# Performance work log

Hardware: AMD Instinct MI355X
Metric: run time of the kernel (lower is better)

## Reference

```python
import jax, jax.numpy as jnp
import numpy as np

N_NODES = 100000
N_EDGES = 300000
HID = 256
N0, N1, N2 = 40000, 30000, 30000
D0, D1, D2 = 512, 256, 128


def setup_inputs() -> dict:
    key = jax.random.key(0)
    ks = jax.random.split(key, 14)
    s = 0.05  # init scale
    return {
        "feat0": jax.random.normal(ks[0], (N0, D0), jnp.float32),
        "feat1": jax.random.normal(ks[1], (N1, D1), jnp.float32),
        "feat2": jax.random.normal(ks[2], (N2, D2), jnp.float32),
        # per-type Linear(in_dim, HID) params (torch Linear: y = x @ W.T + b)
        "fc_w0": jax.random.normal(ks[3], (HID, D0), jnp.float32) * s,
        "fc_b0": jnp.zeros((HID,), jnp.float32),
        "fc_w1": jax.random.normal(ks[4], (HID, D1), jnp.float32) * s,
        "fc_b1": jnp.zeros((HID,), jnp.float32),
        "fc_w2": jax.random.normal(ks[5], (HID, D2), jnp.float32) * s,
        "fc_b2": jnp.zeros((HID,), jnp.float32),
        # GraphConv 1: weight=False, bias=True
        "gc1_bias": jnp.zeros((HID,), jnp.float32),
        # GraphConv 2: weight (in,out) + bias (DGL convention: feat @ W)
        "gc2_weight": jax.random.normal(ks[6], (HID, HID), jnp.float32) * s,
        "gc2_bias": jnp.zeros((HID,), jnp.float32),
        "semantic_weight": jax.random.normal(ks[7], (1, 5), jnp.float32),
        "src": jax.random.randint(ks[8], (N_EDGES,), 0, N_NODES, jnp.int64),
        "dst": jax.random.randint(ks[9], (N_EDGES,), 0, N_NODES, jnp.int64),
    }


def reference(feat0, feat1, feat2, fc_w0, fc_b0, fc_w1, fc_b1, fc_w2, fc_b2,
              gc1_bias, gc2_weight, gc2_bias, semantic_weight, src, dst):
    # per-type projection then concat along node dim -> [N_NODES, HID]
    h = jnp.concatenate([
        feat0 @ fc_w0.T + fc_b0,
        feat1 @ fc_w1.T + fc_b1,
        feat2 @ fc_w2.T + fc_b2,
    ], axis=0)

    ones = jnp.ones((src.shape[0],), h.dtype)
    deg_out = jnp.maximum(jax.ops.segment_sum(ones, src, num_segments=N_NODES), 1.0)
    deg_in = jnp.maximum(jax.ops.segment_sum(ones, dst, num_segments=N_NODES), 1.0)
    norm_out = jax.lax.rsqrt(deg_out)[:, None]  # D_out^{-1/2}
    norm_in = jax.lax.rsqrt(deg_in)[:, None]    # D_in^{-1/2}

    def gconv(x, W, b):
        # DGL GraphConv, norm='both': D_in^{-1/2} A D_out^{-1/2} x W + b, relu
        msg = (x * norm_out)[src]                                  # [E, HID]
        agg = jax.ops.segment_sum(msg, dst, num_segments=N_NODES)  # [N, HID]
        agg = agg * norm_in
        if W is not None:
            agg = agg @ W
        return jax.nn.relu(agg + b)

    # dropout is identity in eval mode
    h = gconv(h, None, gc1_bias)        # layer 0: weight=False
    h = gconv(h, gc2_weight, gc2_bias)  # layer 1
    return h, semantic_weight
```

## Files before the change

### kernel.cpp

```cpp
#include <hip/hip_runtime.h>
#include <cstdint>

#define HID 256
static constexpr int    NNODES = 100000;
static constexpr int    NEDGES = 300000;
static constexpr size_t NH     = (size_t)NNODES * HID;
static constexpr int    SCAN_B = 256;
static constexpr int    NSBLK  = (NNODES + SCAN_B - 1) / SCAN_B;

typedef __attribute__((ext_vector_type(8))) short bf16x8;
typedef __attribute__((ext_vector_type(4))) float f32x4;

__device__ __forceinline__ unsigned short f2bf(float x) {
    unsigned int u = __float_as_uint(x);
    u += 0x7fffu + ((u >> 16) & 1u);
    return (unsigned short)(u >> 16);
}
__device__ __forceinline__ unsigned int pack2(float a, float b) {
    return (unsigned int)f2bf(a) | ((unsigned int)f2bf(b) << 16);
}
__device__ __forceinline__ float bflo(unsigned int u) { return __uint_as_float(u << 16); }
__device__ __forceinline__ float bfhi(unsigned int u) { return __uint_as_float(u & 0xffff0000u); }

__global__ void zero_i32_k(int* __restrict__ p, int n) {
    int i = blockIdx.x * blockDim.x + threadIdx.x;
    if (i < n) p[i] = 0;
}

__global__ void count_deg_k(const int* __restrict__ src, const int* __restrict__ dst,
                            int* __restrict__ degout, int* __restrict__ degin) {
    int e = blockIdx.x * blockDim.x + threadIdx.x;
    if (e < NEDGES) {
        atomicAdd(degout + src[e], 1);
        atomicAdd(degin  + dst[e], 1);
    }
}

__global__ void cvt_weights_k(const float* __restrict__ w0, const float* __restrict__ w1,
                              const float* __restrict__ w2, const float* __restrict__ wg,
                              unsigned short* __restrict__ o0, unsigned short* __restrict__ o1,
                              unsigned short* __restrict__ o2, unsigned short* __restrict__ ogT) {
    int b = blockIdx.x, t = threadIdx.x;
    const float* in; unsigned short* out; int i;
    if (b < 128)      { in = w0; out = o0; i = b * 256 + t; }
    else if (b < 192) { in = w1; out = o1; i = (b - 128) * 256 + t; }
    else if (b < 224) { in = w2; out = o2; i = (b - 192) * 256 + t; }
    else {
        int n = b - 224, k = t;
        ogT[n * 256 + k] = f2bf(wg[k * 256 + n]);
        return;
    }
    float4 v = ((const float4*)in)[i];
    ushort4 w;
    w.x = f2bf(v.x); w.y = f2bf(v.y); w.z = f2bf(v.z); w.w = f2bf(v.w);
    ((ushort4*)out)[i] = w;
}

__global__ void scan_a_k(const int* __restrict__ degin, const int* __restrict__ degout,
                         int* __restrict__ row_off, int* __restrict__ bsums,
                         float* __restrict__ nout, float* __restrict__ nin,
                         const float* __restrict__ sw, float* __restrict__ tail) {
    __shared__ int sm[SCAN_B];
    int t = threadIdx.x;
    int g = blockIdx.x * SCAN_B + t;
    int v = (g < NNODES) ? degin[g] : 0;
    sm[t] = v;
    if (g < NNODES) {
        nout[g] = rsqrtf(fmaxf((float)degout[g], 1.0f));
        nin[g]  = rsqrtf(fmaxf((float)v, 1.0f));
    }
    if (g < 5) tail[g] = sw[g];
    __syncthreads();
#pragma unroll
    for (int off = 1; off < SCAN_B; off <<= 1) {
        int x = (t >= off) ? sm[t - off] : 0;
        __syncthreads();
        sm[t] += x;
        __syncthreads();
    }
    if (g < NNODES) row_off[g] = sm[t] - v;
    if (t == SCAN_B - 1) bsums[blockIdx.x] = sm[t];
}

__global__ void scan_b_k(int* __restrict__ bsums) {
    __shared__ int sm[512];
    int t = threadIdx.x;
    int v = (t < NSBLK) ? bsums[t] : 0;
    sm[t] = v;
    __syncthreads();
#pragma unroll
    for (int off = 1; off < 512; off <<= 1) {
        int x = (t >= off) ? sm[t - off] : 0;
        __syncthreads();
        sm[t] += x;
        __syncthreads();
    }
    if (t < NSBLK) bsums[t] = sm[t] - v;
}

__global__ void scan_c_k(int* __restrict__ row_off, const int* __restrict__ bsums) {
    int g = blockIdx.x * SCAN_B + threadIdx.x;
    if (g < NNODES) row_off[g] += bsums[blockIdx.x];
    if (g == 0) row_off[NNODES] = NEDGES;
}

__global__ void fill_csr_k(const int* __restrict__ src, const int* __restrict__ dst,
                           const int* __restrict__ row_off, int* __restrict__ cursor,
                           int* __restrict__ csr_src) {
    int e = blockIdx.x * blockDim.x + threadIdx.x;
    if (e < NEDGES) {
        int d = dst[e];
        int pos = row_off[d] + atomicAdd(cursor + d, 1);
        csr_src[pos] = src[e];
    }
}

__global__ __launch_bounds__(256) void gather_bf16_k(
    const unsigned short* __restrict__ h, const int* __restrict__ row_off,
    const int* __restrict__ csr_src, const float* __restrict__ nin,
    const float* __restrict__ nout, const float* __restrict__ bias,
    unsigned short* __restrict__ out)
{
    int node = blockIdx.x * 4 + (threadIdx.x >> 6);
    if (node >= NNODES) return;
    int lane = threadIdx.x & 63;
    int beg = row_off[node], end = row_off[node + 1];
    float a0 = 0.f, a1 = 0.f, a2 = 0.f, a3 = 0.f;
    for (int e = beg; e < end; ++e) {
        int s = csr_src[e];
        uint2 v = *(const uint2*)(h + (size_t)s * HID + lane * 4);
        a0 += bflo(v.x); a1 += bfhi(v.x);
        a2 += bflo(v.y); a3 += bfhi(v.y);
    }
    float ni = nin[node], no = nout[node];
    float4 bb = *(const float4*)(bias + lane * 4);
    a0 = fmaxf(fmaf(a0, ni, bb.x), 0.f) * no;
    a1 = fmaxf(fmaf(a1, ni, bb.y), 0.f) * no;
    a2 = fmaxf(fmaf(a2, ni, bb.z), 0.f) * no;
    a3 = fmaxf(fmaf(a3, ni, bb.w), 0.f) * no;
    ushort4 o;
    o.x = f2bf(a0); o.y = f2bf(a1); o.z = f2bf(a2); o.w = f2bf(a3);
    *(ushort4*)(out + (size_t)node * HID + lane * 4) = o;
}

__global__ __launch_bounds__(256, 3) void proj_mfma_k(
    const float* __restrict__ f0, const float* __restrict__ f1, const float* __restrict__ f2,
    const unsigned short* __restrict__ w0, const unsigned short* __restrict__ w1,
    const unsigned short* __restrict__ w2,
    const float* __restrict__ b0, const float* __restrict__ b1, const float* __restrict__ b2,
    const float* __restrict__ nout, unsigned short* __restrict__ h0)
{
    __shared__ unsigned short As[64 * 32];
    __shared__ unsigned short Bs[256 * 32];

    int bx = blockIdx.x;
    const float* A; const unsigned short* B; const float* bias; const float* rs;
    unsigned short* C; int M, K;
    if (bx < 625)       { A = f0; B = w0; bias = b0; rs = nout;          C = h0;                          M = 40000; K = 512; }
    else if (bx < 1094) { bx -= 625;  A = f1; B = w1; bias = b1; rs = nout + 40000; C = h0 + (size_t)40000 * HID; M = 30000; K = 256; }
    else                { bx -= 1094; A = f2; B = w2; bias = b2; rs = nout + 70000; C = h0 + (size_t)70000 * HID; M = 30000; K = 128; }
    const int m0 = bx * 64;

    const int tid  = threadIdx.x;
    const int wn   = tid >> 6;
    const int lane = tid & 63;
    const int half = lane >> 4;
    const int l15  = lane & 15;

    f32x4 acc[4][4];
#pragma unroll
    for (int i = 0; i < 4; ++i)
#pragma unroll
        for (int j = 0; j < 4; ++j)
#pragma unroll
            for (int r = 0; r < 4; ++r) acc[i][j][r] = 0.f;

    const int arow = tid >> 2, ac = tid & 3;
    const int aslot = ac ^ ((arow >> 1) & 3);
    int agm = m0 + arow; if (agm > M - 1) agm = M - 1;

    for (int k0 = 0; k0 < K; k0 += 32) {
        {
            const float* p = A + (size_t)agm * K + k0 + ac * 8;
            float4 v0 = *(const float4*)p;
            float4 v1 = *(const float4*)(p + 4);
            uint4 u;
            u.x = pack2(v0.x, v0.y); u.y = pack2(v0.z, v0.w);
            u.z = pack2(v1.x, v1.y); u.w = pack2(v1.z, v1.w);
            *(uint4*)&As[(arow * 4 + aslot) * 8] = u;
        }
#pragma unroll
        for (int t = 0; t < 4; ++t) {
            int q = tid + t * 256;
            int row = q >> 2, c = q & 3;
            int slot = c ^ ((row >> 1) & 3);
            uint4 v = *(const uint4*)(B + (size_t)row * K + k0 + c * 8);
            *(uint4*)&Bs[(row * 4 + slot) * 8] = v;
        }
        __syncthreads();

        bf16x8 af[4], bfr[4];
#pragma unroll
        for (int i = 0; i < 4; ++i) {
            int m = i * 16 + l15;
            int ca = half ^ ((m >> 1) & 3);
            af[i] = *(const bf16x8*)&As[(m * 4 + ca) * 8];
            int n = wn * 64 + i * 16 + l15;
            int cb = half ^ ((n >> 1) & 3);
            bfr[i] = *(const bf16x8*)&Bs[(n * 4 + cb) * 8];
        }
#pragma unroll
        for (int i = 0; i < 4; ++i)
#pragma unroll
            for (int j = 0; j < 4; ++j)
                acc[i][j] = __builtin_amdgcn_mfma_f32_16x16x32_bf16(
                    af[i], bfr[j], acc[i][j], 0, 0, 0);
        __syncthreads();
    }

    float bj[4];
#pragma unroll
    for (int j = 0; j < 4; ++j) bj[j] = bias[wn * 64 + j * 16 + l15];
#pragma unroll
    for (int i = 0; i < 4; ++i)
#pragma unroll
        for (int r = 0; r < 4; ++r) {
            int m = m0 + i * 16 + (lane >> 4) * 4 + r;
            if (m >= M) continue;
            float rsm = rs[m];
#pragma unroll
            for (int j = 0; j < 4; ++j) {
                int n = wn * 64 + j * 16 + l15;
                C[(size_t)m * HID + n] = f2bf((acc[i][j][r] + bj[j]) * rsm);
            }
        }
}

__global__ __launch_bounds__(256, 3) void final_mfma_k(
    const unsigned short* __restrict__ h1, const int* __restrict__ row_off,
    const int* __restrict__ csr_src, const unsigned short* __restrict__ wT,
    const float* __restrict__ bias, const float* __restrict__ nin,
    float* __restrict__ out)
{
    __shared__ unsigned short As[8 * 64 * 32];
    __shared__ unsigned short Bs[256 * 32];

    const int m0   = blockIdx.x * 64;
    const int tid  = threadIdx.x;
    const int wv   = tid >> 6;
    const int lane = tid & 63;
    const int half = lane >> 4;
    const int l15  = lane & 15;

    {
        const int p   = lane >> 3;
        const int c   = (lane >> 1) & 3;
        const int sub = (lane & 1) * 4;
        for (int r8 = 0; r8 < 16; ++r8) {
            int r = wv * 16 + r8;
            int node = m0 + r; if (node > NNODES - 1) node = NNODES - 1;
            int beg = row_off[node], end = row_off[node + 1];
            float a0 = 0.f, a1 = 0.f, a2 = 0.f, a3 = 0.f;
            for (int e = beg; e < end; ++e) {
                int s = csr_src[e];
                uint2 v = *(const uint2*)(h1 + (size_t)s * HID + lane * 4);
                a0 += bflo(v.x); a1 += bfhi(v.x);
                a2 += bflo(v.y); a3 += bfhi(v.y);
            }
            int slot = c ^ ((r >> 1) & 3);
            ushort4 o;
            o.x = f2bf(a0); o.y = f2bf(a1); o.z = f2bf(a2); o.w = f2bf(a3);
            *(ushort4*)&As[p * 2048 + (r * 4 + slot) * 8 + sub] = o;
        }
    }
    __syncthreads();

    f32x4 acc[4][4];
#pragma unroll
    for (int i = 0; i < 4; ++i)
#pragma unroll
        for (int j = 0; j < 4; ++j)
#pragma unroll
            for (int r = 0; r < 4; ++r) acc[i][j][r] = 0.f;

    const int wn = wv;
    for (int step = 0; step < 8; ++step) {
        int k0 = step * 32;
#pragma unroll
        for (int t = 0; t < 4; ++t) {
            int q = tid + t * 256;
            int row = q >> 2, c = q & 3;
            int slot = c ^ ((row >> 1) & 3);
            uint4 v = *(const uint4*)(wT + (size_t)row * 256 + k0 + c * 8);
            *(uint4*)&Bs[(row * 4 + slot) * 8] = v;
        }
        __syncthreads();

        bf16x8 af[4], bfr[4];
#pragma unroll
        for (int i = 0; i < 4; ++i) {
            int m = i * 16 + l15;
            int ca = half ^ ((m >> 1) & 3);
            af[i] = *(const bf16x8*)&As[step * 2048 + (m * 4 + ca) * 8];
            int n = wn * 64 + i * 16 + l15;
            int cb = half ^ ((n >> 1) & 3);
            bfr[i] = *(const bf16x8*)&Bs[(n * 4 + cb) * 8];
        }
#pragma unroll
        for (int i = 0; i < 4; ++i)
#pragma unroll
            for (int j = 0; j < 4; ++j)
                acc[i][j] = __builtin_amdgcn_mfma_f32_16x16x32_bf16(
                    af[i], bfr[j], acc[i][j], 0, 0, 0);
        __syncthreads();
    }

    float bj[4];
#pragma unroll
    for (int j = 0; j < 4; ++j) bj[j] = bias[wn * 64 + j * 16 + l15];
#pragma unroll
    for (int i = 0; i < 4; ++i)
#pragma unroll
        for (int r = 0; r < 4; ++r) {
            int m = m0 + i * 16 + (lane >> 4) * 4 + r;
            if (m >= NNODES) continue;
            float rsm = nin[m];
#pragma unroll
            for (int j = 0; j < 4; ++j) {
                int n = wn * 64 + j * 16 + l15;
                out[(size_t)m * HID + n] = fmaxf(fmaf(acc[i][j][r], rsm, bj[j]), 0.f);
            }
        }
}

extern "C" void kernel_launch(void* const* d_in, const int* in_sizes, int n_in,
                              void* d_out, int out_size, void* d_ws, size_t ws_size,
                              hipStream_t stream)
{
    const float* feat0    = (const float*)d_in[0];
    const float* feat1    = (const float*)d_in[1];
    const float* feat2    = (const float*)d_in[2];
    const float* fc_w0    = (const float*)d_in[3];
    const float* fc_b0    = (const float*)d_in[4];
    const float* fc_w1    = (const float*)d_in[5];
    const float* fc_b1    = (const float*)d_in[6];
    const float* fc_w2    = (const float*)d_in[7];
    const float* fc_b2    = (const float*)d_in[8];
    const float* gc1_bias = (const float*)d_in[9];
    const float* gc2_w    = (const float*)d_in[10];
    const float* gc2_bias = (const float*)d_in[11];
    const float* sw       = (const float*)d_in[12];
    const int*   src      = (const int*)d_in[13];
    const int*   dst      = (const int*)d_in[14];

    unsigned short* h0b  = (unsigned short*)d_ws;
    unsigned short* h1b  = h0b + NH;
    unsigned short* w0b  = h1b + NH;
    unsigned short* w1b  = w0b + 131072;
    unsigned short* w2b  = w1b + 65536;
    unsigned short* w2Tb = w2b + 32768;
    float* nout = (float*)(w2Tb + 65536);
    float* nin  = nout + NNODES;
    int* deg_out = (int*)(nin + NNODES);
    int* deg_in  = deg_out + NNODES;
    int* cursor  = deg_in + NNODES;
    int* row_off = cursor + NNODES;
    int* bsums   = row_off + NNODES + 1;
    int* csr_src = bsums + 512;
    float* out   = (float*)d_out;

    zero_i32_k<<<(3 * NNODES + 255) / 256, 256, 0, stream>>>(deg_out, 3 * NNODES);
    cvt_weights_k<<<480, 256, 0, stream>>>(fc_w0, fc_w1, fc_w2, gc2_w,
                                           w0b, w1b, w2b, w2Tb);
    count_deg_k<<<(NEDGES + 255) / 256, 256, 0, stream>>>(src, dst, deg_out, deg_in);
    scan_a_k<<<NSBLK, SCAN_B, 0, stream>>>(deg_in, deg_out, row_off, bsums,
                                           nout, nin, sw, out + NH);
    scan_b_k<<<1, 512, 0, stream>>>(bsums);
    scan_c_k<<<NSBLK, SCAN_B, 0, stream>>>(row_off, bsums);
    fill_csr_k<<<(NEDGES + 255) / 256, 256, 0, stream>>>(src, dst, row_off, cursor, csr_src);

    proj_mfma_k<<<1563, 256, 0, stream>>>(feat0, feat1, feat2, w0b, w1b, w2b,
                                          fc_b0, fc_b1, fc_b2, nout, h0b);

    gather_bf16_k<<<(NNODES + 3) / 4, 256, 0, stream>>>(h0b, row_off, csr_src,
                                                        nin, nout, gc1_bias, h1b);

    final_mfma_k<<<(NNODES + 63) / 64, 256, 0, stream>>>(h1b, row_off, csr_src, w2Tb,
                                                         gc2_bias, nin, out);
}
```

Measured before the change: 464.7 us.

## Reorder layer-2 as matmul-then-aggregate and batch gather index loads

Layer 2 now uses the identity A(XW) = (AX)W. The layer-1 epilogue (norm_in, bias, relu, norm_out) moves into the A-tile load of a plain MFMA kernel, which projects first. A separate gather kernel then aggregates the projected rows and applies the final norm, bias and relu in fp32. The gather loop now loads 64 CSR indices per wave at once, broadcasts them with shuffles and unrolls by 4 so several row loads are in flight together. This adds one more kernel launch and a bf16 round-trip of the projected features, in exchange for removing the serialized per-row gather from inside the MFMA kernel.

```diff
diff --git a/kernel.cpp b/kernel.cpp
--- a/kernel.cpp
+++ b/kernel.cpp
@@ -115,32 +115,56 @@
     }
 }
 
-__global__ __launch_bounds__(256) void gather_bf16_k(
+template <int EPI>
+__global__ __launch_bounds__(256) void gather_k(
     const unsigned short* __restrict__ h, const int* __restrict__ row_off,
     const int* __restrict__ csr_src, const float* __restrict__ nin,
-    const float* __restrict__ nout, const float* __restrict__ bias,
-    unsigned short* __restrict__ out)
+    const float* __restrict__ bias, void* __restrict__ outv)
 {
     int node = blockIdx.x * 4 + (threadIdx.x >> 6);
     if (node >= NNODES) return;
     int lane = threadIdx.x & 63;
     int beg = row_off[node], end = row_off[node + 1];
     float a0 = 0.f, a1 = 0.f, a2 = 0.f, a3 = 0.f;
-    for (int e = beg; e < end; ++e) {
-        int s = csr_src[e];
-        uint2 v = *(const uint2*)(h + (size_t)s * HID + lane * 4);
-        a0 += bflo(v.x); a1 += bfhi(v.x);
-        a2 += bflo(v.y); a3 += bfhi(v.y);
-    }
-    float ni = nin[node], no = nout[node];
-    float4 bb = *(const float4*)(bias + lane * 4);
-    a0 = fmaxf(fmaf(a0, ni, bb.x), 0.f) * no;
-    a1 = fmaxf(fmaf(a1, ni, bb.y), 0.f) * no;
-    a2 = fmaxf(fmaf(a2, ni, bb.z), 0.f) * no;
-    a3 = fmaxf(fmaf(a3, ni, bb.w), 0.f) * no;
-    ushort4 o;
-    o.x = f2bf(a0); o.y = f2bf(a1); o.z = f2bf(a2); o.w = f2bf(a3);
-    *(ushort4*)(out + (size_t)node * HID + lane * 4) = o;
+    for (int base = beg; base < end; base += 64) {
+        int cnt = end - base; if (cnt > 64) cnt = 64;
+        int idx = csr_src[base + (lane < cnt ? lane : cnt - 1)];
+        int j = 0;
+        for (; j + 4 <= cnt; j += 4) {
+            int s0 = __shfl(idx, j);
+            int s1 = __shfl(idx, j + 1);
+            int s2 = __shfl(idx, j + 2);
+            int s3 = __shfl(idx, j + 3);
+            uint2 v0 = *(const uint2*)(h + (size_t)s0 * HID + lane * 4);
+            uint2 v1 = *(const uint2*)(h + (size_t)s1 * HID + lane * 4);
+            uint2 v2 = *(const uint2*)(h + (size_t)s2 * HID + lane * 4);
+            uint2 v3 = *(const uint2*)(h + (size_t)s3 * HID + lane * 4);
+            a0 += bflo(v0.x) + bflo(v1.x) + bflo(v2.x) + bflo(v3.x);
+            a1 += bfhi(v0.x) + bfhi(v1.x) + bfhi(v2.x) + bfhi(v3.x);
+            a2 += bflo(v0.y) + bflo(v1.y) + bflo(v2.y) + bflo(v3.y);
+            a3 += bfhi(v0.y) + bfhi(v1.y) + bfhi(v2.y) + bfhi(v3.y);
+        }
+        for (; j < cnt; ++j) {
+            int s = __shfl(idx, j);
+            uint2 v = *(const uint2*)(h + (size_t)s * HID + lane * 4);
+            a0 += bflo(v.x); a1 += bfhi(v.x);
+            a2 += bflo(v.y); a3 += bfhi(v.y);
+        }
+    }
+    if (EPI) {
+        float ni = nin[node];
+        float4 bb = *(const float4*)(bias + lane * 4);
+        float4 o;
+        o.x = fmaxf(fmaf(a0, ni, bb.x), 0.f);
+        o.y = fmaxf(fmaf(a1, ni, bb.y), 0.f);
+        o.z = fmaxf(fmaf(a2, ni, bb.z), 0.f);
+        o.w = fmaxf(fmaf(a3, ni, bb.w), 0.f);
+        *(float4*)((float*)outv + (size_t)node * HID + lane * 4) = o;
+    } else {
+        ushort4 o;
+        o.x = f2bf(a0); o.y = f2bf(a1); o.z = f2bf(a2); o.w = f2bf(a3);
+        *(ushort4*)((unsigned short*)outv + (size_t)node * HID + lane * 4) = o;
+    }
 }
 
 __global__ __launch_bounds__(256, 3) void proj_mfma_k(
@@ -236,45 +260,21 @@
         }
 }
 
-__global__ __launch_bounds__(256, 3) void final_mfma_k(
-    const unsigned short* __restrict__ h1, const int* __restrict__ row_off,
-    const int* __restrict__ csr_src, const unsigned short* __restrict__ wT,
-    const float* __restrict__ bias, const float* __restrict__ nin,
-    float* __restrict__ out)
+__global__ __launch_bounds__(256, 3) void mid_mfma_k(
+    const unsigned short* __restrict__ agg1, const unsigned short* __restrict__ wT,
+    const float* __restrict__ b1, const float* __restrict__ nin,
+    const float* __restrict__ nout, unsigned short* __restrict__ h2)
 {
-    __shared__ unsigned short As[8 * 64 * 32];
+    __shared__ unsigned short As[64 * 32];
     __shared__ unsigned short Bs[256 * 32];
 
     const int m0   = blockIdx.x * 64;
     const int tid  = threadIdx.x;
-    const int wv   = tid >> 6;
+    const int wn   = tid >> 6;
     const int lane = tid & 63;
     const int half = lane >> 4;
     const int l15  = lane & 15;
 
-    {
-        const int p   = lane >> 3;
-        const int c   = (lane >> 1) & 3;
-        const int sub = (lane & 1) * 4;
-        for (int r8 = 0; r8 < 16; ++r8) {
-            int r = wv * 16 + r8;
-            int node = m0 + r; if (node > NNODES - 1) node = NNODES - 1;
-            int beg = row_off[node], end = row_off[node + 1];
-            float a0 = 0.f, a1 = 0.f, a2 = 0.f, a3 = 0.f;
-            for (int e = beg; e < end; ++e) {
-                int s = csr_src[e];
-                uint2 v = *(const uint2*)(h1 + (size_t)s * HID + lane * 4);
-                a0 += bflo(v.x); a1 += bfhi(v.x);
-                a2 += bflo(v.y); a3 += bfhi(v.y);
-            }
-            int slot = c ^ ((r >> 1) & 3);
-            ushort4 o;
-            o.x = f2bf(a0); o.y = f2bf(a1); o.z = f2bf(a2); o.w = f2bf(a3);
-            *(ushort4*)&As[p * 2048 + (r * 4 + slot) * 8 + sub] = o;
-        }
-    }
-    __syncthreads();
-
     f32x4 acc[4][4];
 #pragma unroll
     for (int i = 0; i < 4; ++i)
@@ -283,9 +283,29 @@
 #pragma unroll
             for (int r = 0; r < 4; ++r) acc[i][j][r] = 0.f;
 
-    const int wn = wv;
-    for (int step = 0; step < 8; ++step) {
-        int k0 = step * 32;
+    const int arow = tid >> 2, ac = tid & 3;
+    const int aslot = ac ^ ((arow >> 1) & 3);
+    int agm = m0 + arow; if (agm > NNODES - 1) agm = NNODES - 1;
+    const float ni = nin[agm], no = nout[agm];
+
+    for (int k0 = 0; k0 < 256; k0 += 32) {
+        {
+            uint4 u = *(const uint4*)(agg1 + (size_t)agm * HID + k0 + ac * 8);
+            float4 c0 = *(const float4*)(b1 + k0 + ac * 8);
+            float4 c1 = *(const float4*)(b1 + k0 + ac * 8 + 4);
+            float x0 = fmaxf(fmaf(bflo(u.x), ni, c0.x), 0.f) * no;
+            float x1 = fmaxf(fmaf(bfhi(u.x), ni, c0.y), 0.f) * no;
+            float x2 = fmaxf(fmaf(bflo(u.y), ni, c0.z), 0.f) * no;
+            float x3 = fmaxf(fmaf(bfhi(u.y), ni, c0.w), 0.f) * no;
+            float x4 = fmaxf(fmaf(bflo(u.z), ni, c1.x), 0.f) * no;
+            float x5 = fmaxf(fmaf(bfhi(u.z), ni, c1.y), 0.f) * no;
+            float x6 = fmaxf(fmaf(bflo(u.w), ni, c1.z), 0.f) * no;
+            float x7 = fmaxf(fmaf(bfhi(u.w), ni, c1.w), 0.f) * no;
+            uint4 o;
+            o.x = pack2(x0, x1); o.y = pack2(x2, x3);
+            o.z = pack2(x4, x5); o.w = pack2(x6, x7);
+            *(uint4*)&As[(arow * 4 + aslot) * 8] = o;
+        }
 #pragma unroll
         for (int t = 0; t < 4; ++t) {
             int q = tid + t * 256;
@@ -301,7 +321,7 @@
         for (int i = 0; i < 4; ++i) {
             int m = i * 16 + l15;
             int ca = half ^ ((m >> 1) & 3);
-            af[i] = *(const bf16x8*)&As[step * 2048 + (m * 4 + ca) * 8];
+            af[i] = *(const bf16x8*)&As[(m * 4 + ca) * 8];
             int n = wn * 64 + i * 16 + l15;
             int cb = half ^ ((n >> 1) & 3);
             bfr[i] = *(const bf16x8*)&Bs[(n * 4 + cb) * 8];
@@ -315,20 +335,16 @@
         __syncthreads();
     }
 
-    float bj[4];
-#pragma unroll
-    for (int j = 0; j < 4; ++j) bj[j] = bias[wn * 64 + j * 16 + l15];
 #pragma unroll
     for (int i = 0; i < 4; ++i)
 #pragma unroll
         for (int r = 0; r < 4; ++r) {
             int m = m0 + i * 16 + (lane >> 4) * 4 + r;
             if (m >= NNODES) continue;
-            float rsm = nin[m];
 #pragma unroll
             for (int j = 0; j < 4; ++j) {
                 int n = wn * 64 + j * 16 + l15;
-                out[(size_t)m * HID + n] = fmaxf(fmaf(acc[i][j][r], rsm, bj[j]), 0.f);
+                h2[(size_t)m * HID + n] = f2bf(acc[i][j][r]);
             }
         }
 }
@@ -354,8 +370,9 @@
     const int*   dst      = (const int*)d_in[14];
 
     unsigned short* h0b  = (unsigned short*)d_ws;
-    unsigned short* h1b  = h0b + NH;
-    unsigned short* w0b  = h1b + NH;
+    unsigned short* agg1 = h0b + NH;
+    unsigned short* h2b  = h0b;
+    unsigned short* w0b  = agg1 + NH;
     unsigned short* w1b  = w0b + 131072;
     unsigned short* w2b  = w1b + 65536;
     unsigned short* w2Tb = w2b + 32768;
@@ -382,9 +399,12 @@
     proj_mfma_k<<<1563, 256, 0, stream>>>(feat0, feat1, feat2, w0b, w1b, w2b,
                                           fc_b0, fc_b1, fc_b2, nout, h0b);
 
-    gather_bf16_k<<<(NNODES + 3) / 4, 256, 0, stream>>>(h0b, row_off, csr_src,
-                                                        nin, nout, gc1_bias, h1b);
-
-    final_mfma_k<<<(NNODES + 63) / 64, 256, 0, stream>>>(h1b, row_off, csr_src, w2Tb,
-                                                         gc2_bias, nin, out);
-}
+    gather_k<0><<<(NNODES + 3) / 4, 256, 0, stream>>>(h0b, row_off, csr_src,
+                                                      nullptr, nullptr, agg1);
+
+    mid_mfma_k<<<(NNODES + 63) / 64, 256, 0, stream>>>(agg1, w2Tb, gc1_bias,
+                                                       nin, nout, h2b);
+
+    gather_k<1><<<(NNODES + 3) / 4, 256, 0, stream>>>(h2b, row_off, csr_src,
+                                                      nin, gc2_bias, out);
+}
```

Measured after the change: 404.9 us. 12.9% less time.
